# Optimization experiments

Measured on AMD Instinct MI355X. Metric: run time of the kernel, lower is better.

The kernel has to match this reference:

```python
import jax, jax.numpy as jnp
import numpy as np

MAX_STEP = 4
G_HID = 16      # hidden_graph_num
S_HID = 10      # hidden_graph_size
D = 128         # embed_dim / hidden_dim
N = 100000      # total nodes across batch of session graphs
E = 640000      # total edges
B = 2048        # number of graphs (fixed num_segments)
VOCAB = 100000  # POI vocabulary
NEG_SLOPE = 0.01  # LeakyReLU default


def leaky(x):
    return jnp.where(x >= 0, x, NEG_SLOPE * x)


def setup_inputs() -> dict:
    key = jax.random.key(0)
    ks = jax.random.split(key, 10)
    x_idx = jax.random.randint(ks[0], (N,), 0, VOCAB)
    edge_index = jax.random.randint(ks[1], (2, E), 0, N)
    batch = jnp.sort(jax.random.randint(ks[2], (N,), 0, B))
    poi_emb = jax.random.normal(ks[3], (VOCAB, D), jnp.float32) * 0.02
    fc_w = jax.random.normal(ks[4], (D, D), jnp.float32) / np.sqrt(D)
    fc_b = jnp.zeros((D,), jnp.float32)
    hidden_adj = jax.random.normal(ks[5], (G_HID, S_HID * (S_HID - 1) // 2), jnp.float32)
    hidden_feat = jax.random.normal(ks[6], (G_HID, S_HID, D), jnp.float32)
    mlp_w = jax.random.normal(ks[7], (G_HID * MAX_STEP, D), jnp.float32) / np.sqrt(G_HID * MAX_STEP)
    mlp_b = jnp.zeros((D,), jnp.float32)
    return dict(x_idx=x_idx, edge_index=edge_index, batch=batch,
                poi_emb=poi_emb, fc_w=fc_w, fc_b=fc_b,
                hidden_adj=hidden_adj, hidden_feat=hidden_feat,
                mlp_w=mlp_w, mlp_b=mlp_b)


def reference(x_idx, edge_index, batch, poi_emb, fc_w, fc_b,
              hidden_adj, hidden_feat, mlp_w, mlp_b):
    # Symmetric hidden-graph adjacency from upper-triangular params
    iu, ju = np.triu_indices(S_HID, 1)
    A = jnp.zeros((G_HID, S_HID, S_HID), hidden_adj.dtype).at[:, iu, ju].set(leaky(hidden_adj))
    A = A + jnp.swapaxes(A, 1, 2)

    # Node features: embedding lookup -> Linear -> sigmoid  [N, D]
    x = jax.nn.sigmoid(poi_emb[x_idx] @ fc_w + fc_b)
    z = hidden_feat                                   # [G, S, D]
    zx = jnp.einsum('gsd,nd->gsn', z, x)              # [G, S, N]

    src, dst = edge_index[0], edge_index[1]
    outs = []
    for i in range(MAX_STEP):
        if i == 0:
            # eye @ z == z, so t == zx (faithful to the torch einsum chain)
            t = zx
        else:
            # MessagePassing.propagate with default add aggregation:
            # x_new[v] = sum_{(u->v) in E} x[u]
            x = jax.ops.segment_sum(x[src], dst, num_segments=N)
            z = jnp.einsum('gst,gtd->gsd', A, z)
            t = jnp.einsum('gsd,nd->gsn', z, x)
        t = zx * t                                    # dropout = identity (eval)
        # graph-wise scatter pooling: index_add over node axis -> [B, G, S]
        pooled = jax.ops.segment_sum(jnp.moveaxis(t, 2, 0), batch, num_segments=B)
        outs.append(pooled.sum(axis=2))               # [B, G]

    out = jnp.concatenate(outs, axis=1)               # [B, G*MAX_STEP]
    return leaky(out @ mlp_w + mlp_b)                 # [B, D]
```

## Files before the change

kernel.cpp:

```cpp
#include <hip/hip_runtime.h>
#include <hip/hip_bf16.h>
#include <math.h>

#define G_HID 16
#define S_HID 10
#define D 128
#define MAX_STEP 4
#define NEG 0.01f
#define SCAN_TILE 1024

typedef __attribute__((ext_vector_type(8))) short short8;
typedef __attribute__((ext_vector_type(4))) float f32x4;

__device__ __forceinline__ float leaky_f(float v){ return v >= 0.f ? v : NEG*v; }
__device__ __forceinline__ unsigned short f2bf(float f){
    unsigned int u = __float_as_uint(f);
    u = (u + 0x7FFFu + ((u>>16)&1u)) >> 16;
    return (unsigned short)u;
}
__device__ __forceinline__ float bf_lo(unsigned int v){ return __uint_as_float(v << 16); }
__device__ __forceinline__ float bf_hi(unsigned int v){ return __uint_as_float(v & 0xFFFF0000u); }

__global__ void prep_kernel(const float* __restrict__ hidden_adj,
                            const float* __restrict__ hidden_feat,
                            short* __restrict__ zpack)
{
    int g = blockIdx.x;
    __shared__ float Ag[S_HID][S_HID];
    __shared__ float zb[2][S_HID][D];
    int t = threadIdx.x;
    if (t < S_HID*S_HID) {
        int i = t / S_HID, j = t % S_HID;
        float v = 0.f;
        if (i < j) {
            int idx = 9*i - i*(i-1)/2 + (j - i - 1);
            v = leaky_f(hidden_adj[g*45 + idx]);
        } else if (i > j) {
            int idx = 9*j - j*(j-1)/2 + (i - j - 1);
            v = leaky_f(hidden_adj[g*45 + idx]);
        }
        Ag[i][j] = v;
    }
    for (int idx = t; idx < S_HID*D; idx += 128) {
        int s = idx / D, d = idx % D;
        zb[0][s][d] = hidden_feat[(g*S_HID + s)*D + d];
    }
    __syncthreads();
    int cur = 0;
    for (int step = 0; step < MAX_STEP; ++step) {
        if (step > 0) {
            int nxt = cur ^ 1;
            for (int idx = t; idx < S_HID*D; idx += 128) {
                int s = idx / D, d = idx % D;
                float acc = 0.f;
                #pragma unroll
                for (int u = 0; u < S_HID; ++u) acc += Ag[s][u] * zb[cur][u][d];
                zb[nxt][s][d] = acc;
            }
            cur = nxt;
            __syncthreads();
        }
        for (int idx = t; idx < S_HID*D; idx += 128) {
            int s = idx / D, k = idx % D;
            int row = g*S_HID + s;
            int tt = row >> 4, li = row & 15;
            int kt = k >> 5, q = (k >> 3) & 3, j = k & 7;
            zpack[(((step*10 + tt)*4 + kt)*64 + q*16 + li)*8 + j] = (short)f2bf(zb[cur][s][k]);
        }
        __syncthreads();
    }
}

__global__ void wpack_kernel(const float* __restrict__ fc_w, short* __restrict__ wp){
    int idx = blockIdx.x*256 + threadIdx.x;
    if (idx >= 16384) return;
    int j = idx & 7, lane = (idx >> 3) & 63, ctkt = idx >> 9;
    int ct = ctkt & 7, kt = ctkt >> 3;
    int k   = kt*32 + (lane >> 4)*8 + j;
    int col = ct*16 + (lane & 15);
    wp[idx] = (short)f2bf(fc_w[k*D + col]);
}

__global__ __launch_bounds__(256) void embed_mfma_kernel(const int* __restrict__ x_idx,
                                    const float* __restrict__ poi_emb,
                                    const short* __restrict__ wp,
                                    const float* __restrict__ fc_b,
                                    unsigned short* __restrict__ x0, int N)
{
    __shared__ __align__(16) unsigned short emb[64*136];
    int n0 = blockIdx.x * 64;
    int t = threadIdx.x;
    #pragma unroll
    for (int i = 0; i < 8; ++i) {
        int idx = t + i*256;
        int row = idx >> 5, c4 = (idx & 31)*4;
        int gn = n0 + row;
        float4 v = make_float4(0.f,0.f,0.f,0.f);
        if (gn < N) v = *reinterpret_cast<const float4*>(&poi_emb[(size_t)x_idx[gn]*D + c4]);
        unsigned int p0 = (unsigned int)f2bf(v.x) | ((unsigned int)f2bf(v.y) << 16);
        unsigned int p1 = (unsigned int)f2bf(v.z) | ((unsigned int)f2bf(v.w) << 16);
        *reinterpret_cast<uint2*>(&emb[row*136 + c4]) = make_uint2(p0, p1);
    }
    __syncthreads();
    int l = t & 63, w = t >> 6, li = l & 15, q = l >> 4;
    short8 a[4];
    #pragma unroll
    for (int kt = 0; kt < 4; ++kt)
        a[kt] = *reinterpret_cast<const short8*>(&emb[(w*16 + li)*136 + kt*32 + q*8]);
    f32x4 acc[8];
    #pragma unroll
    for (int ct = 0; ct < 8; ++ct) acc[ct] = (f32x4){0.f,0.f,0.f,0.f};
    #pragma unroll
    for (int kt = 0; kt < 4; ++kt){
        #pragma unroll
        for (int ct = 0; ct < 8; ++ct){
            short8 b = reinterpret_cast<const short8*>(wp)[(kt*8 + ct)*64 + l];
            acc[ct] = __builtin_amdgcn_mfma_f32_16x16x32_bf16(a[kt], b, acc[ct], 0, 0, 0);
        }
    }
    __syncthreads();
    #pragma unroll
    for (int ct = 0; ct < 8; ++ct){
        float bias = fc_b[ct*16 + li];
        #pragma unroll
        for (int r = 0; r < 4; ++r){
            float v = acc[ct][r] + bias;
            float s = 1.f/(1.f + __expf(-v));
            emb[(w*16 + q*4 + r)*136 + ct*16 + li] = f2bf(s);
        }
    }
    __syncthreads();
    int row = t >> 2, ch = t & 3, gn = n0 + row;
    if (gn < N){
        #pragma unroll
        for (int i2 = 0; i2 < 4; ++i2){
            uint4 v = *reinterpret_cast<const uint4*>(&emb[row*136 + ch*32 + i2*8]);
            *reinterpret_cast<uint4*>(&x0[(size_t)gn*D + ch*32 + i2*8]) = v;
        }
    }
}

__global__ void count_kernel(const int* __restrict__ dst, int* __restrict__ offsets, int E){
    int e = blockIdx.x*blockDim.x + threadIdx.x;
    if (e < E) atomicAdd(&offsets[dst[e]+1], 1);
}

__global__ void scan1_kernel(int* __restrict__ data, int* __restrict__ bsums, int n){
    __shared__ int wsum[4];
    int base = blockIdx.x * SCAN_TILE + threadIdx.x*4;
    int v[4];
    #pragma unroll
    for (int j=0;j<4;++j) v[j] = (base+j < n) ? data[base+j] : 0;
    v[1]+=v[0]; v[2]+=v[1]; v[3]+=v[2];
    int lane = threadIdx.x & 63;
    int w = threadIdx.x >> 6;
    int s = v[3];
    for (int d=1; d<64; d<<=1){
        int o = __shfl_up(s, d);
        if (lane >= d) s += o;
    }
    if (lane == 63) wsum[w] = s;
    int sexc = s - v[3];
    __syncthreads();
    int woff = 0;
    for (int ww=0; ww<w; ++ww) woff += wsum[ww];
    int off = woff + sexc;
    #pragma unroll
    for (int j=0;j<4;++j) { if (base+j < n) data[base+j] = v[j] + off; }
    if (threadIdx.x == 255) bsums[blockIdx.x] = off + v[3];
}

__global__ void scan2_kernel(int* __restrict__ bsums, int nb){
    __shared__ int ws[4];
    __shared__ int carry_s;
    if (threadIdx.x == 0) carry_s = 0;
    __syncthreads();
    for (int start = 0; start < nb; start += 256){
        int i = start + (int)threadIdx.x;
        int v = (i < nb) ? bsums[i] : 0;
        int lane = threadIdx.x & 63, w = threadIdx.x >> 6;
        int s = v;
        for (int d=1; d<64; d<<=1){ int o = __shfl_up(s, d); if (lane >= d) s += o; }
        if (lane == 63) ws[w] = s;
        __syncthreads();
        int woff = 0;
        for (int ww=0; ww<w; ++ww) woff += ws[ww];
        int inc = s + woff + carry_s;
        if (i < nb) bsums[i] = inc - v;
        __syncthreads();
        if (threadIdx.x == 255) carry_s = inc;
        __syncthreads();
    }
}

__global__ void scan3_kernel(int* __restrict__ data, const int* __restrict__ bsums, int n){
    int base = blockIdx.x * SCAN_TILE + threadIdx.x*4;
    int add = bsums[blockIdx.x];
    #pragma unroll
    for (int j=0;j<4;++j){ if (base+j < n) data[base+j] += add; }
}

__global__ void fill_kernel(const int* __restrict__ src, const int* __restrict__ dst,
                            const int* __restrict__ offsets, int* __restrict__ fillcnt,
                            int* __restrict__ csr, int E){
    int e = blockIdx.x*blockDim.x + threadIdx.x;
    if (e < E){
        int d = dst[e];
        int pos = atomicAdd(&fillcnt[d], 1);
        csr[offsets[d]+pos] = src[e];
    }
}

__global__ __launch_bounds__(256) void prop_kernel(const unsigned short* __restrict__ xin,
                            unsigned short* __restrict__ xout,
                            const int* __restrict__ offsets, const int* __restrict__ csr, int N){
    int wid = (blockIdx.x*256 + threadIdx.x) >> 6;
    int lane = threadIdx.x & 63;
    if (wid >= N) return;
    int beg = offsets[wid];
    int end = offsets[wid+1];
    int q = lane >> 4;
    int c = lane & 15;
    float acc[8];
    #pragma unroll
    for (int j=0;j<8;++j) acc[j] = 0.f;
    const uint4* xi4 = (const uint4*)xin;
    for (int base = beg; base < end; base += 64){
        int cnt = min(64, end - base);
        int myu = (base + lane < end) ? csr[base + lane] : 0;
        for (int ei = 0; ei < cnt; ei += 8){
            int eqa = ei + q;
            int ua = __shfl(myu, eqa);
            uint4 va = xi4[(size_t)ua*16 + c];
            bool haveB = (ei + 4) < cnt;
            uint4 vb = make_uint4(0,0,0,0);
            if (haveB){
                int eqb = ei + 4 + q;
                int ub = __shfl(myu, eqb & 63);
                vb = xi4[(size_t)ub*16 + c];
                if (eqb >= cnt){ vb.x = vb.y = vb.z = vb.w = 0; }
            }
            if (eqa >= cnt){ va.x = va.y = va.z = va.w = 0; }
            acc[0] += bf_lo(va.x) + bf_lo(vb.x);
            acc[1] += bf_hi(va.x) + bf_hi(vb.x);
            acc[2] += bf_lo(va.y) + bf_lo(vb.y);
            acc[3] += bf_hi(va.y) + bf_hi(vb.y);
            acc[4] += bf_lo(va.z) + bf_lo(vb.z);
            acc[5] += bf_hi(va.z) + bf_hi(vb.z);
            acc[6] += bf_lo(va.w) + bf_lo(vb.w);
            acc[7] += bf_hi(va.w) + bf_hi(vb.w);
        }
    }
    #pragma unroll
    for (int j=0;j<8;++j){
        acc[j] += __shfl_xor(acc[j], 16);
        acc[j] += __shfl_xor(acc[j], 32);
    }
    if (q == 0){
        uint4 o;
        o.x = (unsigned int)f2bf(acc[0]) | ((unsigned int)f2bf(acc[1]) << 16);
        o.y = (unsigned int)f2bf(acc[2]) | ((unsigned int)f2bf(acc[3]) << 16);
        o.z = (unsigned int)f2bf(acc[4]) | ((unsigned int)f2bf(acc[5]) << 16);
        o.w = (unsigned int)f2bf(acc[6]) | ((unsigned int)f2bf(acc[7]) << 16);
        ((uint4*)xout)[(size_t)wid*16 + c] = o;
    }
}

template<int STEP0>
__global__ __launch_bounds__(256) void step_mfma_kernel(const unsigned short* __restrict__ x,
                                 const short* __restrict__ zstep,
                                 const int* __restrict__ batch,
                                 uint2* __restrict__ y0buf,
                                 float* __restrict__ pooled,
                                 int N, int stepoff)
{
    __shared__ __align__(16) char lbuf[42240];
    __shared__ float accs[64][G_HID];
    __shared__ int slots[64];
    __shared__ int slotb[64];
    __shared__ int nslots_s;
    short* zls = (short*)lbuf;
    float* Pf  = (float*)lbuf;
    int n0 = blockIdx.x * 64;
    int t = threadIdx.x;

    #pragma unroll
    for (int i = 0; i < 10; ++i)
        ((uint4*)lbuf)[t + i*256] = ((const uint4*)zstep)[t + i*256];
    #pragma unroll
    for (int i = 0; i < 4; ++i) ((float*)accs)[t + i*256] = 0.f;
    if (t < 64) {
        int gn = n0 + t;
        int b = (gn < N) ? batch[gn] : -1;
        int bprev = -1;
        if (t > 0) bprev = (gn-1 < N) ? batch[gn-1] : -1;
        int flag = (t == 0 || b != bprev) ? 1 : 0;
        int s = flag;
        for (int d=1; d<64; d<<=1){ int o = __shfl_up(s, d); if (t >= d) s += o; }
        int slot = s - 1;
        slots[t] = slot;
        if (flag) slotb[slot] = b;
        if (t == 63) nslots_s = s;
    }
    __syncthreads();

    int l = t & 63, w = t >> 6, li = l & 15, q = l >> 4;
    int node = n0 + w*16 + li;
    bool valid = node < N;
    short8 bw[4];
    #pragma unroll
    for (int kt = 0; kt < 4; ++kt){
        if (valid) bw[kt] = *reinterpret_cast<const short8*>(&x[(size_t)node*D + kt*32 + q*8]);
        else       bw[kt] = (short8){0,0,0,0,0,0,0,0};
    }
    f32x4 accA[10];
    #pragma unroll
    for (int t10 = 0; t10 < 10; ++t10){
        f32x4 acc = (f32x4){0.f,0.f,0.f,0.f};
        #pragma unroll
        for (int kt = 0; kt < 4; ++kt){
            short8 az = *reinterpret_cast<const short8*>(&zls[((t10*4 + kt)*64 + l)*8]);
            acc = __builtin_amdgcn_mfma_f32_16x16x32_bf16(az, bw[kt], acc, 0, 0, 0);
        }
        accA[t10] = acc;
    }
    __syncthreads();

    size_t ybase = ((size_t)blockIdx.x*4 + w)*10*64 + l;
    #pragma unroll
    for (int t10 = 0; t10 < 10; ++t10){
        f32x4 acc = accA[t10];
        float p0, p1, p2, p3;
        if (STEP0){
            uint2 st;
            st.x = (unsigned int)f2bf(acc[0]) | ((unsigned int)f2bf(acc[1]) << 16);
            st.y = (unsigned int)f2bf(acc[2]) | ((unsigned int)f2bf(acc[3]) << 16);
            y0buf[ybase + (size_t)t10*64] = st;
            p0 = acc[0]*acc[0]; p1 = acc[1]*acc[1]; p2 = acc[2]*acc[2]; p3 = acc[3]*acc[3];
        } else {
            uint2 v = y0buf[ybase + (size_t)t10*64];
            p0 = acc[0]*bf_lo(v.x); p1 = acc[1]*bf_hi(v.x);
            p2 = acc[2]*bf_lo(v.y); p3 = acc[3]*bf_hi(v.y);
        }
        int rb = (t10*16 + q*4)*66 + w*16 + li;
        Pf[rb]       = p0;
        Pf[rb + 66]  = p1;
        Pf[rb + 132] = p2;
        Pf[rb + 198] = p3;
    }
    __syncthreads();

    #pragma unroll
    for (int i = 0; i < 4; ++i){
        int g = t & 15, nd = (t >> 4) + i*16;
        float c = 0.f;
        #pragma unroll
        for (int s = 0; s < S_HID; ++s) c += Pf[(g*10 + s)*66 + nd];
        atomicAdd(&accs[slots[nd]][g], c);
    }
    __syncthreads();
    int ns = nslots_s;
    for (int idx = t; idx < ns*G_HID; idx += 256){
        int j = idx >> 4, g = idx & 15;
        int b = slotb[j];
        if (b >= 0) atomicAdd(&pooled[(size_t)b*64 + stepoff + g], accs[j][g]);
    }
}

__global__ void out_kernel(const float* __restrict__ pooled, const float* __restrict__ mlp_w,
                           const float* __restrict__ mlp_b, float* __restrict__ out, int B){
    __shared__ float row[64];
    int b = blockIdx.x;
    int t = threadIdx.x;
    if (t < 64) row[t] = pooled[(size_t)b*64 + t];
    __syncthreads();
    float acc = mlp_b[t];
    for (int j=0;j<64;++j) acc += row[j]*mlp_w[j*D + t];
    out[(size_t)b*D + t] = leaky_f(acc);
}

extern "C" void kernel_launch(void* const* d_in, const int* in_sizes, int n_in,
                              void* d_out, int out_size, void* d_ws, size_t ws_size,
                              hipStream_t stream)
{
    const int*   x_idx = (const int*)d_in[0];
    const int*   edge  = (const int*)d_in[1];
    const int*   batch = (const int*)d_in[2];
    const float* poi   = (const float*)d_in[3];
    const float* fc_w  = (const float*)d_in[4];
    const float* fc_b  = (const float*)d_in[5];
    const float* adj   = (const float*)d_in[6];
    const float* feat  = (const float*)d_in[7];
    const float* mlp_w = (const float*)d_in[8];
    const float* mlp_b = (const float*)d_in[9];
    float* out = (float*)d_out;

    int N = in_sizes[0];
    int E = in_sizes[1] / 2;
    int B = out_size / D;
    int sblk = (N + 63) / 64;
    size_t NP = (size_t)sblk * 64;

    char* p = (char*)d_ws;
    auto alloc = [&](size_t bytes)->char* {
        char* r = p;
        p += (bytes + 255) & ~(size_t)255;
        return r;
    };
    unsigned short* x0 = (unsigned short*)alloc(NP*D*2);
    unsigned short* xa = (unsigned short*)alloc(NP*D*2);
    unsigned short* xb = (unsigned short*)alloc(NP*D*2);
    uint2* y0buf       = (uint2*)alloc(NP*160*2);
    float* pooled      = (float*)alloc((size_t)B*64*4);
    short* zpack       = (short*)alloc((size_t)MAX_STEP*20480*2);
    short* wp          = (short*)alloc((size_t)16384*2);
    int*   offsets     = (int*)alloc((size_t)(N+1)*4);
    int*   fillcnt     = (int*)alloc((size_t)N*4);
    int*   csr         = (int*)alloc((size_t)E*4);
    int*   bsums       = (int*)alloc(4096);

    const int* srcp = edge;
    const int* dstp = edge + E;

    hipMemsetAsync(offsets, 0, (size_t)(N+1)*4, stream);
    hipMemsetAsync(fillcnt, 0, (size_t)N*4, stream);
    hipMemsetAsync(pooled, 0, (size_t)B*64*4, stream);

    prep_kernel<<<G_HID, 128, 0, stream>>>(adj, feat, zpack);
    wpack_kernel<<<64, 256, 0, stream>>>(fc_w, wp);
    embed_mfma_kernel<<<sblk, 256, 0, stream>>>(x_idx, poi, wp, fc_b, x0, N);

    count_kernel<<<(E+255)/256, 256, 0, stream>>>(dstp, offsets, E);
    int scan_n = N + 1;
    int nblk = (scan_n + SCAN_TILE - 1) / SCAN_TILE;
    scan1_kernel<<<nblk, 256, 0, stream>>>(offsets, bsums, scan_n);
    scan2_kernel<<<1, 256, 0, stream>>>(bsums, nblk);
    scan3_kernel<<<nblk, 256, 0, stream>>>(offsets, bsums, scan_n);
    fill_kernel<<<(E+255)/256, 256, 0, stream>>>(srcp, dstp, offsets, fillcnt, csr, E);

    step_mfma_kernel<1><<<sblk, 256, 0, stream>>>(x0, zpack, batch, y0buf, pooled, N, 0);

    const unsigned short* xin = x0;
    unsigned short* bufs[2] = {xa, xb};
    for (int i = 1; i < MAX_STEP; ++i){
        unsigned short* xout = bufs[(i-1) & 1];
        prop_kernel<<<(N+3)/4, 256, 0, stream>>>(xin, xout, offsets, csr, N);
        step_mfma_kernel<0><<<sblk, 256, 0, stream>>>(xout, zpack + (size_t)i*20480, batch,
                                                      y0buf, pooled, N, i*G_HID);
        xin = xout;
    }
    out_kernel<<<B, D, 0, stream>>>(pooled, mlp_w, mlp_b, out, B);
}
```

Baseline: 323.8 us.

## Fuse embedding with step-0 pooling and restructure per-graph z packing

Merges the embedding/Linear/sigmoid kernel into the step-0 kernel, so the freshly computed node features feed the z·x MFMA without a separate launch or a global reload. The z packing now pads each hidden graph to 16 rows, and the step kernels loop per graph, reading z fragments directly from global memory instead of staging them in LDS. Per-node partial sums go to LDS through atomics instead of the large Pf transpose buffer. The CSR fill uses a device-to-device copy of the offsets as its cursor, which removes one memset and one indirection. In exchange, padding raises MFMA work from 10 to 16 row tiles per step, and the step kernels take many more LDS atomics.

```diff
diff --git a/kernel.cpp b/kernel.cpp
--- a/kernel.cpp
+++ b/kernel.cpp
@@ -8,6 +8,7 @@
 #define MAX_STEP 4
 #define NEG 0.01f
 #define SCAN_TILE 1024
+#define ZSTEP_ELEMS (16*4*64*8)
 
 typedef __attribute__((ext_vector_type(8))) short short8;
 typedef __attribute__((ext_vector_type(4))) float f32x4;
@@ -60,12 +61,11 @@
             cur = nxt;
             __syncthreads();
         }
-        for (int idx = t; idx < S_HID*D; idx += 128) {
-            int s = idx / D, k = idx % D;
-            int row = g*S_HID + s;
-            int tt = row >> 4, li = row & 15;
+        for (int idx = t; idx < 16*D; idx += 128) {
+            int s = idx >> 7, k = idx & 127;
+            float v = (s < S_HID) ? zb[cur][s][k] : 0.f;
             int kt = k >> 5, q = (k >> 3) & 3, j = k & 7;
-            zpack[(((step*10 + tt)*4 + kt)*64 + q*16 + li)*8 + j] = (short)f2bf(zb[cur][s][k]);
+            zpack[(size_t)step*ZSTEP_ELEMS + ((g*4 + kt)*64 + q*16 + s)*8 + j] = (short)f2bf(v);
         }
         __syncthreads();
     }
@@ -79,65 +79,6 @@
     int k   = kt*32 + (lane >> 4)*8 + j;
     int col = ct*16 + (lane & 15);
     wp[idx] = (short)f2bf(fc_w[k*D + col]);
-}
-
-__global__ __launch_bounds__(256) void embed_mfma_kernel(const int* __restrict__ x_idx,
-                                    const float* __restrict__ poi_emb,
-                                    const short* __restrict__ wp,
-                                    const float* __restrict__ fc_b,
-                                    unsigned short* __restrict__ x0, int N)
-{
-    __shared__ __align__(16) unsigned short emb[64*136];
-    int n0 = blockIdx.x * 64;
-    int t = threadIdx.x;
-    #pragma unroll
-    for (int i = 0; i < 8; ++i) {
-        int idx = t + i*256;
-        int row = idx >> 5, c4 = (idx & 31)*4;
-        int gn = n0 + row;
-        float4 v = make_float4(0.f,0.f,0.f,0.f);
-        if (gn < N) v = *reinterpret_cast<const float4*>(&poi_emb[(size_t)x_idx[gn]*D + c4]);
-        unsigned int p0 = (unsigned int)f2bf(v.x) | ((unsigned int)f2bf(v.y) << 16);
-        unsigned int p1 = (unsigned int)f2bf(v.z) | ((unsigned int)f2bf(v.w) << 16);
-        *reinterpret_cast<uint2*>(&emb[row*136 + c4]) = make_uint2(p0, p1);
-    }
-    __syncthreads();
-    int l = t & 63, w = t >> 6, li = l & 15, q = l >> 4;
-    short8 a[4];
-    #pragma unroll
-    for (int kt = 0; kt < 4; ++kt)
-        a[kt] = *reinterpret_cast<const short8*>(&emb[(w*16 + li)*136 + kt*32 + q*8]);
-    f32x4 acc[8];
-    #pragma unroll
-    for (int ct = 0; ct < 8; ++ct) acc[ct] = (f32x4){0.f,0.f,0.f,0.f};
-    #pragma unroll
-    for (int kt = 0; kt < 4; ++kt){
-        #pragma unroll
-        for (int ct = 0; ct < 8; ++ct){
-            short8 b = reinterpret_cast<const short8*>(wp)[(kt*8 + ct)*64 + l];
-            acc[ct] = __builtin_amdgcn_mfma_f32_16x16x32_bf16(a[kt], b, acc[ct], 0, 0, 0);
-        }
-    }
-    __syncthreads();
-    #pragma unroll
-    for (int ct = 0; ct < 8; ++ct){
-        float bias = fc_b[ct*16 + li];
-        #pragma unroll
-        for (int r = 0; r < 4; ++r){
-            float v = acc[ct][r] + bias;
-            float s = 1.f/(1.f + __expf(-v));
-            emb[(w*16 + q*4 + r)*136 + ct*16 + li] = f2bf(s);
-        }
-    }
-    __syncthreads();
-    int row = t >> 2, ch = t & 3, gn = n0 + row;
-    if (gn < N){
-        #pragma unroll
-        for (int i2 = 0; i2 < 4; ++i2){
-            uint4 v = *reinterpret_cast<const uint4*>(&emb[row*136 + ch*32 + i2*8]);
-            *reinterpret_cast<uint4*>(&x0[(size_t)gn*D + ch*32 + i2*8]) = v;
-        }
-    }
 }
 
 __global__ void count_kernel(const int* __restrict__ dst, int* __restrict__ offsets, int E){
@@ -201,13 +142,12 @@
 }
 
 __global__ void fill_kernel(const int* __restrict__ src, const int* __restrict__ dst,
-                            const int* __restrict__ offsets, int* __restrict__ fillcnt,
-                            int* __restrict__ csr, int E){
+                            int* __restrict__ cursor, int* __restrict__ csr, int E){
     int e = blockIdx.x*blockDim.x + threadIdx.x;
     if (e < E){
         int d = dst[e];
-        int pos = atomicAdd(&fillcnt[d], 1);
-        csr[offsets[d]+pos] = src[e];
+        int pos = atomicAdd(&cursor[d], 1);
+        csr[pos] = src[e];
     }
 }
 
@@ -266,29 +206,8 @@
     }
 }
 
-template<int STEP0>
-__global__ __launch_bounds__(256) void step_mfma_kernel(const unsigned short* __restrict__ x,
-                                 const short* __restrict__ zstep,
-                                 const int* __restrict__ batch,
-                                 uint2* __restrict__ y0buf,
-                                 float* __restrict__ pooled,
-                                 int N, int stepoff)
-{
-    __shared__ __align__(16) char lbuf[42240];
-    __shared__ float accs[64][G_HID];
-    __shared__ int slots[64];
-    __shared__ int slotb[64];
-    __shared__ int nslots_s;
-    short* zls = (short*)lbuf;
-    float* Pf  = (float*)lbuf;
-    int n0 = blockIdx.x * 64;
-    int t = threadIdx.x;
-
-    #pragma unroll
-    for (int i = 0; i < 10; ++i)
-        ((uint4*)lbuf)[t + i*256] = ((const uint4*)zstep)[t + i*256];
-    #pragma unroll
-    for (int i = 0; i < 4; ++i) ((float*)accs)[t + i*256] = 0.f;
+__device__ __forceinline__ void compute_slots(const int* __restrict__ batch, int n0, int N,
+                                              int* slots, int* slotb, int* nslots_s, int t){
     if (t < 64) {
         int gn = n0 + t;
         int b = (gn < N) ? batch[gn] : -1;
@@ -300,71 +219,183 @@
         int slot = s - 1;
         slots[t] = slot;
         if (flag) slotb[slot] = b;
-        if (t == 63) nslots_s = s;
-    }
+        if (t == 63) *nslots_s = s;
+    }
+}
+
+template<int STEP0>
+__device__ __forceinline__ void step_phase(const short8 bw[4],
+        const short* __restrict__ zstep,
+        float (*accs)[G_HID], const int* slots,
+        unsigned short* __restrict__ y0buf,
+        int node, bool valid, int t)
+{
+    int l = t & 63, w = t >> 6, q = l >> 4, node16 = l & 15;
+    unsigned int* y32 = (unsigned int*)y0buf;
+    #pragma unroll
+    for (int g = 0; g < G_HID; ++g){
+        f32x4 acc = (f32x4){0.f,0.f,0.f,0.f};
+        #pragma unroll
+        for (int kt = 0; kt < 4; ++kt){
+            short8 az = *reinterpret_cast<const short8*>(&zstep[((g*4 + kt)*64 + l)*8]);
+            acc = __builtin_amdgcn_mfma_f32_16x16x32_bf16(az, bw[kt], acc, 0, 0, 0);
+        }
+        size_t yw = ((size_t)node*160 + g*10 + q*4) >> 1;
+        float p0=0.f, p1=0.f, p2=0.f, p3=0.f;
+        if (STEP0){
+            if (valid){
+                if (q < 2){
+                    y32[yw]   = (unsigned int)f2bf(acc[0]) | ((unsigned int)f2bf(acc[1]) << 16);
+                    y32[yw+1] = (unsigned int)f2bf(acc[2]) | ((unsigned int)f2bf(acc[3]) << 16);
+                } else if (q == 2){
+                    y32[yw]   = (unsigned int)f2bf(acc[0]) | ((unsigned int)f2bf(acc[1]) << 16);
+                }
+            }
+            p0 = acc[0]*acc[0]; p1 = acc[1]*acc[1]; p2 = acc[2]*acc[2]; p3 = acc[3]*acc[3];
+        } else {
+            if (valid){
+                if (q < 2){
+                    unsigned int v0 = y32[yw], v1 = y32[yw+1];
+                    p0 = acc[0]*bf_lo(v0); p1 = acc[1]*bf_hi(v0);
+                    p2 = acc[2]*bf_lo(v1); p3 = acc[3]*bf_hi(v1);
+                } else if (q == 2){
+                    unsigned int v0 = y32[yw];
+                    p0 = acc[0]*bf_lo(v0); p1 = acc[1]*bf_hi(v0);
+                }
+            }
+        }
+        float c = p0 + p1 + p2 + p3;
+        c += __shfl_xor(c, 16);
+        c += __shfl_xor(c, 32);
+        if (l < 16 && valid) atomicAdd(&accs[w*16 + node16][g], c);
+    }
+}
+
+__device__ __forceinline__ void flush_pooled(float (*accs)[G_HID], const int* slots,
+        const int* slotb, int nslots, float* __restrict__ pooled, int stepoff, int t){
+    __shared__ float sacc[64][G_HID];
+    for (int idx = t; idx < 64*G_HID; idx += 256) ((float*)sacc)[idx] = 0.f;
+    __syncthreads();
+    #pragma unroll
+    for (int i = 0; i < 4; ++i){
+        int nd = (t >> 4) + i*16, g = t & 15;
+        atomicAdd(&sacc[slots[nd]][g], accs[nd][g]);
+    }
+    __syncthreads();
+    for (int idx = t; idx < nslots*G_HID; idx += 256){
+        int j = idx >> 4, g = idx & 15;
+        int b = slotb[j];
+        if (b >= 0) atomicAdd(&pooled[(size_t)b*64 + stepoff + g], sacc[j][g]);
+    }
+}
+
+__global__ __launch_bounds__(256) void embed_step0_kernel(
+        const int* __restrict__ x_idx, const float* __restrict__ poi_emb,
+        const short* __restrict__ wp, const float* __restrict__ fc_b,
+        const short* __restrict__ zstep, const int* __restrict__ batch,
+        unsigned short* __restrict__ x0, unsigned short* __restrict__ y0buf,
+        float* __restrict__ pooled, int N)
+{
+    __shared__ __align__(16) unsigned short xs[64*136];
+    __shared__ float accs[64][G_HID];
+    __shared__ int slots[64];
+    __shared__ int slotb[64];
+    __shared__ int nslots_s;
+    int n0 = blockIdx.x * 64;
+    int t = threadIdx.x;
+
+    #pragma unroll
+    for (int i = 0; i < 8; ++i) {
+        int idx = t + i*256;
+        int row = idx >> 5, c4 = (idx & 31)*4;
+        int gn = n0 + row;
+        float4 v = make_float4(0.f,0.f,0.f,0.f);
+        if (gn < N) v = *reinterpret_cast<const float4*>(&poi_emb[(size_t)x_idx[gn]*D + c4]);
+        unsigned int p0 = (unsigned int)f2bf(v.x) | ((unsigned int)f2bf(v.y) << 16);
+        unsigned int p1 = (unsigned int)f2bf(v.z) | ((unsigned int)f2bf(v.w) << 16);
+        *reinterpret_cast<uint2*>(&xs[row*136 + c4]) = make_uint2(p0, p1);
+    }
+    for (int idx = t; idx < 64*G_HID; idx += 256) ((float*)accs)[idx] = 0.f;
+    compute_slots(batch, n0, N, slots, slotb, &nslots_s, t);
     __syncthreads();
 
     int l = t & 63, w = t >> 6, li = l & 15, q = l >> 4;
+    short8 a[4];
+    #pragma unroll
+    for (int kt = 0; kt < 4; ++kt)
+        a[kt] = *reinterpret_cast<const short8*>(&xs[(w*16 + li)*136 + kt*32 + q*8]);
+    f32x4 facc[8];
+    #pragma unroll
+    for (int ct = 0; ct < 8; ++ct) facc[ct] = (f32x4){0.f,0.f,0.f,0.f};
+    #pragma unroll
+    for (int kt = 0; kt < 4; ++kt){
+        #pragma unroll
+        for (int ct = 0; ct < 8; ++ct){
+            short8 b = reinterpret_cast<const short8*>(wp)[(kt*8 + ct)*64 + l];
+            facc[ct] = __builtin_amdgcn_mfma_f32_16x16x32_bf16(a[kt], b, facc[ct], 0, 0, 0);
+        }
+    }
+    #pragma unroll
+    for (int ct = 0; ct < 8; ++ct){
+        float bias = fc_b[ct*16 + li];
+        #pragma unroll
+        for (int r = 0; r < 4; ++r){
+            int row = w*16 + q*4 + r;
+            float s = (n0 + row < N) ? 1.f/(1.f + __expf(-(facc[ct][r] + bias))) : 0.f;
+            xs[row*136 + ct*16 + li] = f2bf(s);
+        }
+    }
+    __syncthreads();
+    {
+        int row = t >> 2, ch = t & 3, gn = n0 + row;
+        if (gn < N){
+            #pragma unroll
+            for (int i2 = 0; i2 < 4; ++i2){
+                uint4 v = *reinterpret_cast<const uint4*>(&xs[row*136 + ch*32 + i2*8]);
+                *reinterpret_cast<uint4*>(&x0[(size_t)gn*D + ch*32 + i2*8]) = v;
+            }
+        }
+    }
     int node = n0 + w*16 + li;
     bool valid = node < N;
     short8 bw[4];
     #pragma unroll
+    for (int kt = 0; kt < 4; ++kt)
+        bw[kt] = *reinterpret_cast<const short8*>(&xs[(w*16 + li)*136 + kt*32 + q*8]);
+
+    step_phase<1>(bw, zstep, accs, slots, y0buf, node, valid, t);
+    __syncthreads();
+    flush_pooled(accs, slots, slotb, nslots_s, pooled, 0, t);
+}
+
+__global__ __launch_bounds__(256) void step_kernel2(
+        const unsigned short* __restrict__ x,
+        const short* __restrict__ zstep, const int* __restrict__ batch,
+        unsigned short* __restrict__ y0buf, float* __restrict__ pooled,
+        int N, int stepoff)
+{
+    __shared__ float accs[64][G_HID];
+    __shared__ int slots[64];
+    __shared__ int slotb[64];
+    __shared__ int nslots_s;
+    int n0 = blockIdx.x * 64;
+    int t = threadIdx.x;
+    for (int idx = t; idx < 64*G_HID; idx += 256) ((float*)accs)[idx] = 0.f;
+    compute_slots(batch, n0, N, slots, slotb, &nslots_s, t);
+    __syncthreads();
+
+    int l = t & 63, w = t >> 6, q = l >> 4, node16 = l & 15;
+    int node = n0 + w*16 + node16;
+    bool valid = node < N;
+    short8 bw[4];
+    #pragma unroll
     for (int kt = 0; kt < 4; ++kt){
         if (valid) bw[kt] = *reinterpret_cast<const short8*>(&x[(size_t)node*D + kt*32 + q*8]);
         else       bw[kt] = (short8){0,0,0,0,0,0,0,0};
     }
-    f32x4 accA[10];
-    #pragma unroll
-    for (int t10 = 0; t10 < 10; ++t10){
-        f32x4 acc = (f32x4){0.f,0.f,0.f,0.f};
-        #pragma unroll
-        for (int kt = 0; kt < 4; ++kt){
-            short8 az = *reinterpret_cast<const short8*>(&zls[((t10*4 + kt)*64 + l)*8]);
-            acc = __builtin_amdgcn_mfma_f32_16x16x32_bf16(az, bw[kt], acc, 0, 0, 0);
-        }
-        accA[t10] = acc;
-    }
-    __syncthreads();
-
-    size_t ybase = ((size_t)blockIdx.x*4 + w)*10*64 + l;
-    #pragma unroll
-    for (int t10 = 0; t10 < 10; ++t10){
-        f32x4 acc = accA[t10];
-        float p0, p1, p2, p3;
-        if (STEP0){
-            uint2 st;
-            st.x = (unsigned int)f2bf(acc[0]) | ((unsigned int)f2bf(acc[1]) << 16);
-            st.y = (unsigned int)f2bf(acc[2]) | ((unsigned int)f2bf(acc[3]) << 16);
-            y0buf[ybase + (size_t)t10*64] = st;
-            p0 = acc[0]*acc[0]; p1 = acc[1]*acc[1]; p2 = acc[2]*acc[2]; p3 = acc[3]*acc[3];
-        } else {
-            uint2 v = y0buf[ybase + (size_t)t10*64];
-            p0 = acc[0]*bf_lo(v.x); p1 = acc[1]*bf_hi(v.x);
-            p2 = acc[2]*bf_lo(v.y); p3 = acc[3]*bf_hi(v.y);
-        }
-        int rb = (t10*16 + q*4)*66 + w*16 + li;
-        Pf[rb]       = p0;
-        Pf[rb + 66]  = p1;
-        Pf[rb + 132] = p2;
-        Pf[rb + 198] = p3;
-    }
-    __syncthreads();
-
-    #pragma unroll
-    for (int i = 0; i < 4; ++i){
-        int g = t & 15, nd = (t >> 4) + i*16;
-        float c = 0.f;
-        #pragma unroll
-        for (int s = 0; s < S_HID; ++s) c += Pf[(g*10 + s)*66 + nd];
-        atomicAdd(&accs[slots[nd]][g], c);
-    }
-    __syncthreads();
-    int ns = nslots_s;
-    for (int idx = t; idx < ns*G_HID; idx += 256){
-        int j = idx >> 4, g = idx & 15;
-        int b = slotb[j];
-        if (b >= 0) atomicAdd(&pooled[(size_t)b*64 + stepoff + g], accs[j][g]);
-    }
+    step_phase<0>(bw, zstep, accs, slots, y0buf, node, valid, t);
+    __syncthreads();
+    flush_pooled(accs, slots, slotb, nslots_s, pooled, stepoff, t);
 }
 
 __global__ void out_kernel(const float* __restrict__ pooled, const float* __restrict__ mlp_w,
@@ -410,12 +441,12 @@
     unsigned short* x0 = (unsigned short*)alloc(NP*D*2);
     unsigned short* xa = (unsigned short*)alloc(NP*D*2);
     unsigned short* xb = (unsigned short*)alloc(NP*D*2);
-    uint2* y0buf       = (uint2*)alloc(NP*160*2);
+    unsigned short* y0buf = (unsigned short*)alloc(NP*160*2);
     float* pooled      = (float*)alloc((size_t)B*64*4);
-    short* zpack       = (short*)alloc((size_t)MAX_STEP*20480*2);
+    short* zpack       = (short*)alloc((size_t)MAX_STEP*ZSTEP_ELEMS*2);
     short* wp          = (short*)alloc((size_t)16384*2);
     int*   offsets     = (int*)alloc((size_t)(N+1)*4);
-    int*   fillcnt     = (int*)alloc((size_t)N*4);
+    int*   cursor      = (int*)alloc((size_t)N*4);
     int*   csr         = (int*)alloc((size_t)E*4);
     int*   bsums       = (int*)alloc(4096);
 
@@ -423,12 +454,10 @@
     const int* dstp = edge + E;
 
     hipMemsetAsync(offsets, 0, (size_t)(N+1)*4, stream);
-    hipMemsetAsync(fillcnt, 0, (size_t)N*4, stream);
     hipMemsetAsync(pooled, 0, (size_t)B*64*4, stream);
 
     prep_kernel<<<G_HID, 128, 0, stream>>>(adj, feat, zpack);
     wpack_kernel<<<64, 256, 0, stream>>>(fc_w, wp);
-    embed_mfma_kernel<<<sblk, 256, 0, stream>>>(x_idx, poi, wp, fc_b, x0, N);
 
     count_kernel<<<(E+255)/256, 256, 0, stream>>>(dstp, offsets, E);
     int scan_n = N + 1;
@@ -436,17 +465,19 @@
     scan1_kernel<<<nblk, 256, 0, stream>>>(offsets, bsums, scan_n);
     scan2_kernel<<<1, 256, 0, stream>>>(bsums, nblk);
     scan3_kernel<<<nblk, 256, 0, stream>>>(offsets, bsums, scan_n);
-    fill_kernel<<<(E+255)/256, 256, 0, stream>>>(srcp, dstp, offsets, fillcnt, csr, E);
-
-    step_mfma_kernel<1><<<sblk, 256, 0, stream>>>(x0, zpack, batch, y0buf, pooled, N, 0);
+    hipMemcpyAsync(cursor, offsets, (size_t)N*4, hipMemcpyDeviceToDevice, stream);
+    fill_kernel<<<(E+255)/256, 256, 0, stream>>>(srcp, dstp, cursor, csr, E);
+
+    embed_step0_kernel<<<sblk, 256, 0, stream>>>(x_idx, poi, wp, fc_b, zpack, batch,
+                                                 x0, y0buf, pooled, N);
 
     const unsigned short* xin = x0;
     unsigned short* bufs[2] = {xa, xb};
     for (int i = 1; i < MAX_STEP; ++i){
         unsigned short* xout = bufs[(i-1) & 1];
         prop_kernel<<<(N+3)/4, 256, 0, stream>>>(xin, xout, offsets, csr, N);
-        step_mfma_kernel<0><<<sblk, 256, 0, stream>>>(xout, zpack + (size_t)i*20480, batch,
-                                                      y0buf, pooled, N, i*G_HID);
+        step_kernel2<<<sblk, 256, 0, stream>>>(xout, zpack + (size_t)i*ZSTEP_ELEMS, batch,
+                                               y0buf, pooled, N, i*G_HID);
         xin = xout;
     }
     out_kernel<<<B, D, 0, stream>>>(pooled, mlp_w, mlp_b, out, B);
```

After: 382.5 us. 1.18x slower.
